# Performance work log

Hardware: AMD Instinct MI355X
Metric: run time of the kernel (lower is better)

The kernel has to match this reference:

```python
import jax, jax.numpy as jnp
import numpy as np

N_VARS = 2_000_000
N_CONSTRS = 1_000_000
NNZ = 20_000_000  # ~20 nonzeros per constraint


def setup_inputs() -> dict:
    key = jax.random.key(0)
    k = jax.random.split(key, 6)
    pred = jax.random.normal(k[0], (N_VARS,), dtype=jnp.float32)
    constr_idx = jax.random.randint(k[1], (NNZ,), 0, N_CONSTRS)
    var_idx = jax.random.randint(k[2], (NNZ,), 0, N_VARS)
    coeff = jax.random.normal(k[3], (NNZ,), dtype=jnp.float32)
    constr_rhs = jax.random.normal(k[4], (N_CONSTRS,), dtype=jnp.float32)
    # sense: 1 = <=, 2 = >=, 3 = ==
    constr_sense = jax.random.randint(k[5], (N_CONSTRS,), 1, 4)
    return {
        "pred": pred,
        "constr_idx": constr_idx,
        "var_idx": var_idx,
        "coeff": coeff,
        "constr_rhs": constr_rhs,
        "constr_sense": constr_sense,
        "n_vars": N_VARS,
        "n_constrs": N_CONSTRS,
    }


def reference(pred, constr_idx, var_idx, coeff, constr_rhs, constr_sense, n_vars, n_constrs):
    # var_types is None -> all binary: values = sigmoid(pred)
    values = jax.nn.sigmoid(pred)
    # COO sparse matvec: ax[c] = sum over nonzeros with constr_idx==c of coeff * values[var_idx]
    ax = jax.ops.segment_sum(coeff * values[var_idx], constr_idx, num_segments=n_constrs)
    diff = ax - constr_rhs
    zero = jnp.zeros((), dtype=diff.dtype)
    violations = jnp.where(
        constr_sense == 1, jnp.maximum(diff, zero),          # <= : relu(ax - b)
        jnp.where(
            constr_sense == 2, jnp.maximum(-diff, zero),     # >= : relu(b - ax)
            jnp.where(constr_sense == 3, jnp.abs(diff), zero)  # == : |ax - b|
        ),
    )
    return violations.mean()  # reduction='mean'
```

## Files before the change

kernel.cpp:

```cpp
#include <hip/hip_runtime.h>
#include <hip/hip_fp16.h>


#define BW_LOG2 13
#define BW (1 << BW_LOG2)
#define MAXNB 128
#define NREP 8
#define P1_THREADS 512
#define VPT 8
#define P1_CHUNK (P1_THREADS * VPT)
#define CUR_PAD 16

typedef int   v4i __attribute__((ext_vector_type(4)));
typedef float v4f __attribute__((ext_vector_type(4)));

__global__ void sigmoid_kernel(const float* __restrict__ pred,
                               __half* __restrict__ values, int n) {
    int i = blockIdx.x * blockDim.x + threadIdx.x;
    int stride = gridDim.x * blockDim.x;
    int n4 = n >> 2;
    const v4f* p4 = (const v4f*)pred;
    uint2* o = (uint2*)values;
    for (int j = i; j < n4; j += stride) {
        v4f p = p4[j];
        float a0 = 1.0f / (1.0f + __expf(-p.x));
        float a1 = 1.0f / (1.0f + __expf(-p.y));
        float a2 = 1.0f / (1.0f + __expf(-p.z));
        float a3 = 1.0f / (1.0f + __expf(-p.w));
        unsigned lo = ((unsigned)__half_as_ushort(__float2half_rn(a1)) << 16) |
                      (unsigned)__half_as_ushort(__float2half_rn(a0));
        unsigned hi = ((unsigned)__half_as_ushort(__float2half_rn(a3)) << 16) |
                      (unsigned)__half_as_ushort(__float2half_rn(a2));
        o[j] = make_uint2(lo, hi);
    }
    for (int j = (n4 << 2) + i; j < n; j += stride)
        values[j] = __float2half_rn(1.0f / (1.0f + __expf(-pred[j])));
}

__global__ __launch_bounds__(P1_THREADS) void binning_kernel(
    const int* __restrict__ cidx, const int* __restrict__ vidx,
    const float* __restrict__ coeff, const __half* __restrict__ values,
    unsigned long long* __restrict__ bins, int* __restrict__ cursor,
    float* __restrict__ ovf, int nnz, int nb, int cap) {
    __shared__ int hist[MAXNB];
    __shared__ int sbase[MAXNB];
    const int tid = threadIdx.x;
    const long long start = (long long)blockIdx.x * P1_CHUNK;

    for (int i = tid; i < nb; i += P1_THREADS) hist[i] = 0;
    __syncthreads();

    unsigned packed[VPT];
    float val[VPT];

    if (start + P1_CHUNK <= (long long)nnz) {
        const v4i* c4 = (const v4i*)(cidx + start);
        const v4i* v4 = (const v4i*)(vidx + start);
        const v4f* w4 = (const v4f*)(coeff + start);
#pragma unroll
        for (int k = 0; k < VPT / 4; ++k) {
            int g = k * P1_THREADS + tid;
            v4i c = __builtin_nontemporal_load(&c4[g]);
            v4i v = __builtin_nontemporal_load(&v4[g]);
            v4f w = __builtin_nontemporal_load(&w4[g]);
            float x0 = w.x * __half2float(values[v.x]);
            float x1 = w.y * __half2float(values[v.y]);
            float x2 = w.z * __half2float(values[v.z]);
            float x3 = w.w * __half2float(values[v.w]);
            int l0 = atomicAdd(&hist[c.x >> BW_LOG2], 1);
            int l1 = atomicAdd(&hist[c.y >> BW_LOG2], 1);
            int l2 = atomicAdd(&hist[c.z >> BW_LOG2], 1);
            int l3 = atomicAdd(&hist[c.w >> BW_LOG2], 1);
            packed[k * 4 + 0] = (unsigned)c.x | ((unsigned)l0 << 20);
            packed[k * 4 + 1] = (unsigned)c.y | ((unsigned)l1 << 20);
            packed[k * 4 + 2] = (unsigned)c.z | ((unsigned)l2 << 20);
            packed[k * 4 + 3] = (unsigned)c.w | ((unsigned)l3 << 20);
            val[k * 4 + 0] = x0;
            val[k * 4 + 1] = x1;
            val[k * 4 + 2] = x2;
            val[k * 4 + 3] = x3;
        }
    } else {
#pragma unroll
        for (int k = 0; k < VPT; ++k) {
            long long idx = start + (long long)k * P1_THREADS + tid;
            if (idx < nnz) {
                int c = cidx[idx];
                float x = coeff[idx] * __half2float(values[vidx[idx]]);
                int l = atomicAdd(&hist[c >> BW_LOG2], 1);
                packed[k] = (unsigned)c | ((unsigned)l << 20);
                val[k] = x;
            } else {
                packed[k] = 0xFFFFFFFFu;
            }
        }
    }
    __syncthreads();
    for (int i = tid; i < nb; i += P1_THREADS)
        sbase[i] = atomicAdd(&cursor[i * CUR_PAD], hist[i]);
    __syncthreads();
#pragma unroll
    for (int k = 0; k < VPT; ++k) {
        if (packed[k] == 0xFFFFFFFFu) continue;
        unsigned c = packed[k] & 0xFFFFFu;
        int loc = (int)(packed[k] >> 20);
        int b = (int)(c >> BW_LOG2);
        int pos = sbase[b] + loc;
        if (pos < cap) {
            unsigned long long e = (unsigned long long)c |
                ((unsigned long long)__float_as_uint(val[k]) << 32);
            bins[(size_t)b * cap + pos] = e;
        } else {
            atomicAdd(&ovf[c], val[k]);
        }
    }
}

__global__ __launch_bounds__(512) void bucket_accum_kernel(
    const unsigned long long* __restrict__ bins, const int* __restrict__ cursor,
    float* __restrict__ rep, int nb, int cap, int n_constrs, int rep_stride) {
    __shared__ float acc[BW];
    const int tid = threadIdx.x;
    const int b = blockIdx.x >> 3;
    const int r = blockIdx.x & 7;

    v4f* a4 = (v4f*)acc;
    v4f zero = {0.0f, 0.0f, 0.0f, 0.0f};
#pragma unroll
    for (int k = 0; k < BW / 4 / 512; ++k)
        a4[k * 512 + tid] = zero;
    __syncthreads();

    int cnt = cursor[b * CUR_PAD];
    if (cnt > cap) cnt = cap;
    int begin = (int)((long long)cnt * r / NREP);
    int end = (int)((long long)cnt * (r + 1) / NREP);
    const unsigned long long* mb = bins + (size_t)b * cap;
    const unsigned cbase = (unsigned)b << BW_LOG2;

    int i = begin + tid;
    for (; i + 512 * 3 < end; i += 512 * 4) {
        unsigned long long e0 = mb[i];
        unsigned long long e1 = mb[i + 512];
        unsigned long long e2 = mb[i + 1024];
        unsigned long long e3 = mb[i + 1536];
        atomicAdd(&acc[((unsigned)e0 & 0xFFFFFu) - cbase], __uint_as_float((unsigned)(e0 >> 32)));
        atomicAdd(&acc[((unsigned)e1 & 0xFFFFFu) - cbase], __uint_as_float((unsigned)(e1 >> 32)));
        atomicAdd(&acc[((unsigned)e2 & 0xFFFFFu) - cbase], __uint_as_float((unsigned)(e2 >> 32)));
        atomicAdd(&acc[((unsigned)e3 & 0xFFFFFu) - cbase], __uint_as_float((unsigned)(e3 >> 32)));
    }
    for (; i < end; i += 512) {
        unsigned long long e = mb[i];
        atomicAdd(&acc[((unsigned)e & 0xFFFFFu) - cbase], __uint_as_float((unsigned)(e >> 32)));
    }
    __syncthreads();

    float* out = rep + (size_t)r * rep_stride + cbase;
    int lim = n_constrs - (int)cbase;
    if (lim >= BW) {
        v4f* o4 = (v4f*)out;
#pragma unroll
        for (int k = 0; k < BW / 4 / 512; ++k)
            o4[k * 512 + tid] = a4[k * 512 + tid];
    } else {
        for (int j = tid; j < lim; j += 512) out[j] = acc[j];
    }
}

template <int NR>
__global__ void violation_reduce_kernel(const float* __restrict__ rep,
                                        const float* __restrict__ rhs,
                                        const int* __restrict__ sense,
                                        float* __restrict__ out,
                                        int n, int rep_stride, float inv_n) {
    int i = blockIdx.x * blockDim.x + threadIdx.x;
    int stride = gridDim.x * blockDim.x;
    float acc = 0.0f;
    int n4 = n >> 2;
    const float4* r4 = (const float4*)rhs;
    const int4* s4 = (const int4*)sense;
    for (int j = i; j < n4; j += stride) {
        float4 a = make_float4(0.0f, 0.0f, 0.0f, 0.0f);
#pragma unroll
        for (int r = 0; r < NR; ++r) {
            const float4* a4 = (const float4*)(rep + (size_t)r * (size_t)rep_stride);
            float4 t = a4[j];
            a.x += t.x; a.y += t.y; a.z += t.z; a.w += t.w;
        }
        float4 rr = r4[j];
        int4 s = s4[j];
        float d;
        d = a.x - rr.x;
        acc += (s.x == 1) ? fmaxf(d, 0.0f) : (s.x == 2) ? fmaxf(-d, 0.0f) : (s.x == 3) ? fabsf(d) : 0.0f;
        d = a.y - rr.y;
        acc += (s.y == 1) ? fmaxf(d, 0.0f) : (s.y == 2) ? fmaxf(-d, 0.0f) : (s.y == 3) ? fabsf(d) : 0.0f;
        d = a.z - rr.z;
        acc += (s.z == 1) ? fmaxf(d, 0.0f) : (s.z == 2) ? fmaxf(-d, 0.0f) : (s.z == 3) ? fabsf(d) : 0.0f;
        d = a.w - rr.w;
        acc += (s.w == 1) ? fmaxf(d, 0.0f) : (s.w == 2) ? fmaxf(-d, 0.0f) : (s.w == 3) ? fabsf(d) : 0.0f;
    }
    for (int j = (n4 << 2) + i; j < n; j += stride) {
        float a = 0.0f;
#pragma unroll
        for (int r = 0; r < NR; ++r) a += rep[(size_t)r * (size_t)rep_stride + j];
        float d = a - rhs[j];
        int s = sense[j];
        acc += (s == 1) ? fmaxf(d, 0.0f) : (s == 2) ? fmaxf(-d, 0.0f) : (s == 3) ? fabsf(d) : 0.0f;
    }

    for (int off = 32; off > 0; off >>= 1)
        acc += __shfl_down(acc, off, 64);

    __shared__ float lds[8];
    int lane = threadIdx.x & 63;
    int wave = threadIdx.x >> 6;
    if (lane == 0) lds[wave] = acc;
    __syncthreads();
    if (wave == 0) {
        int nwaves = blockDim.x >> 6;
        float b = (lane < nwaves) ? lds[lane] : 0.0f;
        for (int off = 4; off > 0; off >>= 1)
            b += __shfl_down(b, off, 64);
        if (lane == 0) atomicAdd(out, b * inv_n);
    }
}

__global__ void scatter_kernel(const int* __restrict__ cidx,
                               const int* __restrict__ vidx,
                               const float* __restrict__ coeff,
                               const __half* __restrict__ values,
                               float* __restrict__ ax, int nnz) {
    int i = blockIdx.x * blockDim.x + threadIdx.x;
    int stride = gridDim.x * blockDim.x;
    int n4 = nnz >> 2;
    const int4* c4 = (const int4*)cidx;
    const int4* v4 = (const int4*)vidx;
    const float4* w4 = (const float4*)coeff;
    for (int j = i; j < n4; j += stride) {
        int4 c = c4[j];
        int4 v = v4[j];
        float4 w = w4[j];
        atomicAdd(&ax[c.x], w.x * __half2float(values[v.x]));
        atomicAdd(&ax[c.y], w.y * __half2float(values[v.y]));
        atomicAdd(&ax[c.z], w.z * __half2float(values[v.z]));
        atomicAdd(&ax[c.w], w.w * __half2float(values[v.w]));
    }
    for (int j = (n4 << 2) + i; j < nnz; j += stride)
        atomicAdd(&ax[cidx[j]], coeff[j] * __half2float(values[vidx[j]]));
}

extern "C" void kernel_launch(void* const* d_in, const int* in_sizes, int n_in,
                              void* d_out, int out_size, void* d_ws, size_t ws_size,
                              hipStream_t stream) {
    const float* pred  = (const float*)d_in[0];
    const int*   cidx  = (const int*)d_in[1];
    const int*   vidx  = (const int*)d_in[2];
    const float* coeff = (const float*)d_in[3];
    const float* rhs   = (const float*)d_in[4];
    const int*   sense = (const int*)d_in[5];

    const int n_vars    = in_sizes[0];
    const int nnz       = in_sizes[1];
    const int n_constrs = in_sizes[4];

    const int rep_stride = (n_constrs + 15) & ~15;
    const size_t vh_bytes = ((size_t)n_vars * 2 + 255) & ~(size_t)255;

    __half* values = (__half*)d_ws;
    float* rep = (float*)((char*)d_ws + vh_bytes);
    float* ovf = rep + (size_t)NREP * rep_stride;
    int* cursor = (int*)(ovf + rep_stride);
    unsigned long long* bins =
        (unsigned long long*)(cursor + MAXNB * CUR_PAD);

    const int nb = (n_constrs + BW - 1) >> BW_LOG2;
    long long cap_ll = (long long)nnz * BW / n_constrs
                     + (long long)nnz / ((long long)(nb > 0 ? nb : 1) * 32) + 2048;
    const int cap = (int)cap_ll;
    const size_t need = vh_bytes
                      + (size_t)(NREP + 1) * rep_stride * 4
                      + (size_t)MAXNB * CUR_PAD * 4
                      + (size_t)nb * (size_t)cap * 8;
    const bool fast = (nb >= 1) && (nb <= MAXNB) && (n_constrs < (1 << 20)) &&
                      (nnz > P1_CHUNK) && (ws_size >= need);

    hipMemsetAsync(d_out, 0, sizeof(float), stream);

    {
        int threads = 256;
        int work = n_vars >> 2;
        int blocks = (work + threads - 1) / threads;
        if (blocks < 1) blocks = 1;
        if (blocks > 2048) blocks = 2048;
        sigmoid_kernel<<<blocks, threads, 0, stream>>>(pred, values, n_vars);
    }

    if (fast) {
        hipMemsetAsync(cursor, 0, (size_t)MAXNB * CUR_PAD * sizeof(int), stream);
        hipMemsetAsync(ovf, 0, (size_t)rep_stride * sizeof(float), stream);

        int p1_blocks = (int)(((long long)nnz + P1_CHUNK - 1) / P1_CHUNK);
        binning_kernel<<<p1_blocks, P1_THREADS, 0, stream>>>(
            cidx, vidx, coeff, values, bins, cursor, ovf, nnz, nb, cap);

        bucket_accum_kernel<<<nb * NREP, 512, 0, stream>>>(
            bins, cursor, rep, nb, cap, n_constrs, rep_stride);

        int threads = 256;
        int work = n_constrs >> 2;
        int blocks = (work + threads - 1) / threads;
        if (blocks > 4096) blocks = 4096;
        violation_reduce_kernel<NREP + 1><<<blocks, threads, 0, stream>>>(
            rep, rhs, sense, (float*)d_out, n_constrs, rep_stride,
            1.0f / (float)n_constrs);
    } else {
        hipMemsetAsync(rep, 0, (size_t)n_constrs * sizeof(float), stream);
        int threads = 256;
        int work = nnz >> 2;
        int blocks = (work + threads - 1) / threads;
        if (blocks > 8192) blocks = 8192;
        scatter_kernel<<<blocks, threads, 0, stream>>>(
            cidx, vidx, coeff, values, rep, nnz);

        int vthreads = 256;
        int vwork = n_constrs >> 2;
        int vblocks = (vwork + vthreads - 1) / vthreads;
        if (vblocks > 4096) vblocks = 4096;
        violation_reduce_kernel<1><<<vblocks, vthreads, 0, stream>>>(
            rep, rhs, sense, (float*)d_out, n_constrs, n_constrs,
            1.0f / (float)n_constrs);
    }
}
```

Baseline: 539.6 us.

## Pack bins to 32-bit half entries and fuse accumulation with violation reduction

Bin entries shrink from 64-bit (constraint index plus fp32 value) to 32-bit (12-bit local index plus fp16 product), halving the scatter and readback traffic of the bin array. Bucket width halves to 4096 and block size doubles to 1024, so each bucket is accumulated by one block in LDS. That block then computes the violations and reduces them directly, which removes the replicated partial-sum buffers and the separate violation kernel. The cost is fewer accumulation blocks (about 245), which may underfill the GPU. Storing each product in fp16 also adds rounding error to every term.

Result: faster. 525.8 us (-2.6%).

```diff
diff --git a/kernel.cpp b/kernel.cpp
--- a/kernel.cpp
+++ b/kernel.cpp
@@ -2,11 +2,10 @@
 #include <hip/hip_fp16.h>
 
 
-#define BW_LOG2 13
+#define BW_LOG2 12
 #define BW (1 << BW_LOG2)
-#define MAXNB 128
-#define NREP 8
-#define P1_THREADS 512
+#define MAXNB 256
+#define P1_THREADS 1024
 #define VPT 8
 #define P1_CHUNK (P1_THREADS * VPT)
 #define CUR_PAD 16
@@ -40,7 +39,7 @@
 __global__ __launch_bounds__(P1_THREADS) void binning_kernel(
     const int* __restrict__ cidx, const int* __restrict__ vidx,
     const float* __restrict__ coeff, const __half* __restrict__ values,
-    unsigned long long* __restrict__ bins, int* __restrict__ cursor,
+    unsigned* __restrict__ bins, int* __restrict__ cursor,
     float* __restrict__ ovf, int nnz, int nb, int cap) {
     __shared__ int hist[MAXNB];
     __shared__ int sbase[MAXNB];
@@ -50,8 +49,9 @@
     for (int i = tid; i < nb; i += P1_THREADS) hist[i] = 0;
     __syncthreads();
 
-    unsigned packed[VPT];
-    float val[VPT];
+    int   cc[VPT];
+    float vv[VPT];
+    int   ll[VPT];
 
     if (start + P1_CHUNK <= (long long)nnz) {
         const v4i* c4 = (const v4i*)(cidx + start);
@@ -63,22 +63,16 @@
             v4i c = __builtin_nontemporal_load(&c4[g]);
             v4i v = __builtin_nontemporal_load(&v4[g]);
             v4f w = __builtin_nontemporal_load(&w4[g]);
-            float x0 = w.x * __half2float(values[v.x]);
-            float x1 = w.y * __half2float(values[v.y]);
-            float x2 = w.z * __half2float(values[v.z]);
-            float x3 = w.w * __half2float(values[v.w]);
-            int l0 = atomicAdd(&hist[c.x >> BW_LOG2], 1);
-            int l1 = atomicAdd(&hist[c.y >> BW_LOG2], 1);
-            int l2 = atomicAdd(&hist[c.z >> BW_LOG2], 1);
-            int l3 = atomicAdd(&hist[c.w >> BW_LOG2], 1);
-            packed[k * 4 + 0] = (unsigned)c.x | ((unsigned)l0 << 20);
-            packed[k * 4 + 1] = (unsigned)c.y | ((unsigned)l1 << 20);
-            packed[k * 4 + 2] = (unsigned)c.z | ((unsigned)l2 << 20);
-            packed[k * 4 + 3] = (unsigned)c.w | ((unsigned)l3 << 20);
-            val[k * 4 + 0] = x0;
-            val[k * 4 + 1] = x1;
-            val[k * 4 + 2] = x2;
-            val[k * 4 + 3] = x3;
+            vv[k * 4 + 0] = w.x * __half2float(values[v.x]);
+            vv[k * 4 + 1] = w.y * __half2float(values[v.y]);
+            vv[k * 4 + 2] = w.z * __half2float(values[v.z]);
+            vv[k * 4 + 3] = w.w * __half2float(values[v.w]);
+            cc[k * 4 + 0] = c.x; cc[k * 4 + 1] = c.y;
+            cc[k * 4 + 2] = c.z; cc[k * 4 + 3] = c.w;
+            ll[k * 4 + 0] = atomicAdd(&hist[c.x >> BW_LOG2], 1);
+            ll[k * 4 + 1] = atomicAdd(&hist[c.y >> BW_LOG2], 1);
+            ll[k * 4 + 2] = atomicAdd(&hist[c.z >> BW_LOG2], 1);
+            ll[k * 4 + 3] = atomicAdd(&hist[c.w >> BW_LOG2], 1);
         }
     } else {
 #pragma unroll
@@ -86,12 +80,11 @@
             long long idx = start + (long long)k * P1_THREADS + tid;
             if (idx < nnz) {
                 int c = cidx[idx];
-                float x = coeff[idx] * __half2float(values[vidx[idx]]);
-                int l = atomicAdd(&hist[c >> BW_LOG2], 1);
-                packed[k] = (unsigned)c | ((unsigned)l << 20);
-                val[k] = x;
+                cc[k] = c;
+                vv[k] = coeff[idx] * __half2float(values[vidx[idx]]);
+                ll[k] = atomicAdd(&hist[c >> BW_LOG2], 1);
             } else {
-                packed[k] = 0xFFFFFFFFu;
+                cc[k] = -1;
             }
         }
     }
@@ -101,127 +94,88 @@
     __syncthreads();
 #pragma unroll
     for (int k = 0; k < VPT; ++k) {
-        if (packed[k] == 0xFFFFFFFFu) continue;
-        unsigned c = packed[k] & 0xFFFFFu;
-        int loc = (int)(packed[k] >> 20);
-        int b = (int)(c >> BW_LOG2);
-        int pos = sbase[b] + loc;
+        int c = cc[k];
+        if (c < 0) continue;
+        int b = c >> BW_LOG2;
+        int pos = sbase[b] + ll[k];
         if (pos < cap) {
-            unsigned long long e = (unsigned long long)c |
-                ((unsigned long long)__float_as_uint(val[k]) << 32);
-            bins[(size_t)b * cap + pos] = e;
+            unsigned short hb = __half_as_ushort(__float2half_rn(vv[k]));
+            bins[(size_t)b * cap + pos] =
+                ((unsigned)hb << 16) | (unsigned)(c & (BW - 1));
         } else {
-            atomicAdd(&ovf[c], val[k]);
+            atomicAdd(&ovf[c], vv[k]);
         }
     }
 }
 
-__global__ __launch_bounds__(512) void bucket_accum_kernel(
-    const unsigned long long* __restrict__ bins, const int* __restrict__ cursor,
-    float* __restrict__ rep, int nb, int cap, int n_constrs, int rep_stride) {
+__global__ __launch_bounds__(1024) void accum_viol_kernel(
+    const unsigned* __restrict__ bins, const int* __restrict__ cursor,
+    const float* __restrict__ ovf, const float* __restrict__ rhs,
+    const int* __restrict__ sense, float* __restrict__ out,
+    int cap, int n_constrs, float inv_n) {
     __shared__ float acc[BW];
     const int tid = threadIdx.x;
-    const int b = blockIdx.x >> 3;
-    const int r = blockIdx.x & 7;
-
-    v4f* a4 = (v4f*)acc;
-    v4f zero = {0.0f, 0.0f, 0.0f, 0.0f};
-#pragma unroll
-    for (int k = 0; k < BW / 4 / 512; ++k)
-        a4[k * 512 + tid] = zero;
+    const int b = blockIdx.x;
+
+#pragma unroll
+    for (int k = 0; k < BW / 1024; ++k) acc[k * 1024 + tid] = 0.0f;
     __syncthreads();
 
     int cnt = cursor[b * CUR_PAD];
     if (cnt > cap) cnt = cap;
-    int begin = (int)((long long)cnt * r / NREP);
-    int end = (int)((long long)cnt * (r + 1) / NREP);
-    const unsigned long long* mb = bins + (size_t)b * cap;
-    const unsigned cbase = (unsigned)b << BW_LOG2;
-
-    int i = begin + tid;
-    for (; i + 512 * 3 < end; i += 512 * 4) {
-        unsigned long long e0 = mb[i];
-        unsigned long long e1 = mb[i + 512];
-        unsigned long long e2 = mb[i + 1024];
-        unsigned long long e3 = mb[i + 1536];
-        atomicAdd(&acc[((unsigned)e0 & 0xFFFFFu) - cbase], __uint_as_float((unsigned)(e0 >> 32)));
-        atomicAdd(&acc[((unsigned)e1 & 0xFFFFFu) - cbase], __uint_as_float((unsigned)(e1 >> 32)));
-        atomicAdd(&acc[((unsigned)e2 & 0xFFFFFu) - cbase], __uint_as_float((unsigned)(e2 >> 32)));
-        atomicAdd(&acc[((unsigned)e3 & 0xFFFFFu) - cbase], __uint_as_float((unsigned)(e3 >> 32)));
-    }
-    for (; i < end; i += 512) {
-        unsigned long long e = mb[i];
-        atomicAdd(&acc[((unsigned)e & 0xFFFFFu) - cbase], __uint_as_float((unsigned)(e >> 32)));
-    }
-    __syncthreads();
-
-    float* out = rep + (size_t)r * rep_stride + cbase;
-    int lim = n_constrs - (int)cbase;
-    if (lim >= BW) {
-        v4f* o4 = (v4f*)out;
-#pragma unroll
-        for (int k = 0; k < BW / 4 / 512; ++k)
-            o4[k * 512 + tid] = a4[k * 512 + tid];
-    } else {
-        for (int j = tid; j < lim; j += 512) out[j] = acc[j];
-    }
-}
-
-template <int NR>
-__global__ void violation_reduce_kernel(const float* __restrict__ rep,
-                                        const float* __restrict__ rhs,
-                                        const int* __restrict__ sense,
-                                        float* __restrict__ out,
-                                        int n, int rep_stride, float inv_n) {
-    int i = blockIdx.x * blockDim.x + threadIdx.x;
-    int stride = gridDim.x * blockDim.x;
-    float acc = 0.0f;
-    int n4 = n >> 2;
-    const float4* r4 = (const float4*)rhs;
-    const int4* s4 = (const int4*)sense;
-    for (int j = i; j < n4; j += stride) {
-        float4 a = make_float4(0.0f, 0.0f, 0.0f, 0.0f);
-#pragma unroll
-        for (int r = 0; r < NR; ++r) {
-            const float4* a4 = (const float4*)(rep + (size_t)r * (size_t)rep_stride);
-            float4 t = a4[j];
-            a.x += t.x; a.y += t.y; a.z += t.z; a.w += t.w;
+    const unsigned* mb = bins + (size_t)b * cap;
+
+    int i = tid;
+    for (; i + 1024 * 3 < cnt; i += 1024 * 4) {
+        unsigned e0 = __builtin_nontemporal_load(&mb[i]);
+        unsigned e1 = __builtin_nontemporal_load(&mb[i + 1024]);
+        unsigned e2 = __builtin_nontemporal_load(&mb[i + 2048]);
+        unsigned e3 = __builtin_nontemporal_load(&mb[i + 3072]);
+        atomicAdd(&acc[e0 & (BW - 1)],
+                  __half2float(__ushort_as_half((unsigned short)(e0 >> 16))));
+        atomicAdd(&acc[e1 & (BW - 1)],
+                  __half2float(__ushort_as_half((unsigned short)(e1 >> 16))));
+        atomicAdd(&acc[e2 & (BW - 1)],
+                  __half2float(__ushort_as_half((unsigned short)(e2 >> 16))));
+        atomicAdd(&acc[e3 & (BW - 1)],
+                  __half2float(__ushort_as_half((unsigned short)(e3 >> 16))));
+    }
+    for (; i < cnt; i += 1024) {
+        unsigned e = __builtin_nontemporal_load(&mb[i]);
+        atomicAdd(&acc[e & (BW - 1)],
+                  __half2float(__ushort_as_half((unsigned short)(e >> 16))));
+    }
+    __syncthreads();
+
+    const int cbase = b << BW_LOG2;
+    float sum = 0.0f;
+#pragma unroll
+    for (int k = 0; k < BW / 1024; ++k) {
+        int j = k * 1024 + tid;
+        int c = cbase + j;
+        if (c < n_constrs) {
+            float a = acc[j] + ovf[c];
+            float d = a - rhs[c];
+            int s = sense[c];
+            sum += (s == 1) ? fmaxf(d, 0.0f)
+                 : (s == 2) ? fmaxf(-d, 0.0f)
+                 : (s == 3) ? fabsf(d) : 0.0f;
         }
-        float4 rr = r4[j];
-        int4 s = s4[j];
-        float d;
-        d = a.x - rr.x;
-        acc += (s.x == 1) ? fmaxf(d, 0.0f) : (s.x == 2) ? fmaxf(-d, 0.0f) : (s.x == 3) ? fabsf(d) : 0.0f;
-        d = a.y - rr.y;
-        acc += (s.y == 1) ? fmaxf(d, 0.0f) : (s.y == 2) ? fmaxf(-d, 0.0f) : (s.y == 3) ? fabsf(d) : 0.0f;
-        d = a.z - rr.z;
-        acc += (s.z == 1) ? fmaxf(d, 0.0f) : (s.z == 2) ? fmaxf(-d, 0.0f) : (s.z == 3) ? fabsf(d) : 0.0f;
-        d = a.w - rr.w;
-        acc += (s.w == 1) ? fmaxf(d, 0.0f) : (s.w == 2) ? fmaxf(-d, 0.0f) : (s.w == 3) ? fabsf(d) : 0.0f;
-    }
-    for (int j = (n4 << 2) + i; j < n; j += stride) {
-        float a = 0.0f;
-#pragma unroll
-        for (int r = 0; r < NR; ++r) a += rep[(size_t)r * (size_t)rep_stride + j];
-        float d = a - rhs[j];
-        int s = sense[j];
-        acc += (s == 1) ? fmaxf(d, 0.0f) : (s == 2) ? fmaxf(-d, 0.0f) : (s == 3) ? fabsf(d) : 0.0f;
     }
 
     for (int off = 32; off > 0; off >>= 1)
-        acc += __shfl_down(acc, off, 64);
-
-    __shared__ float lds[8];
-    int lane = threadIdx.x & 63;
-    int wave = threadIdx.x >> 6;
-    if (lane == 0) lds[wave] = acc;
+        sum += __shfl_down(sum, off, 64);
+
+    __shared__ float lds[16];
+    int lane = tid & 63;
+    int wave = tid >> 6;
+    if (lane == 0) lds[wave] = sum;
     __syncthreads();
     if (wave == 0) {
-        int nwaves = blockDim.x >> 6;
-        float b = (lane < nwaves) ? lds[lane] : 0.0f;
-        for (int off = 4; off > 0; off >>= 1)
-            b += __shfl_down(b, off, 64);
-        if (lane == 0) atomicAdd(out, b * inv_n);
+        float v = (lane < 16) ? lds[lane] : 0.0f;
+        for (int off = 8; off > 0; off >>= 1)
+            v += __shfl_down(v, off, 64);
+        if (lane == 0) atomicAdd(out, v * inv_n);
     }
 }
 
@@ -249,6 +203,36 @@
         atomicAdd(&ax[cidx[j]], coeff[j] * __half2float(values[vidx[j]]));
 }
 
+__global__ void violation_reduce_kernel(const float* __restrict__ ax,
+                                        const float* __restrict__ rhs,
+                                        const int* __restrict__ sense,
+                                        float* __restrict__ out,
+                                        int n, float inv_n) {
+    int i = blockIdx.x * blockDim.x + threadIdx.x;
+    int stride = gridDim.x * blockDim.x;
+    float acc = 0.0f;
+    for (int j = i; j < n; j += stride) {
+        float d = ax[j] - rhs[j];
+        int s = sense[j];
+        acc += (s == 1) ? fmaxf(d, 0.0f) : (s == 2) ? fmaxf(-d, 0.0f)
+             : (s == 3) ? fabsf(d) : 0.0f;
+    }
+    for (int off = 32; off > 0; off >>= 1)
+        acc += __shfl_down(acc, off, 64);
+    __shared__ float lds[8];
+    int lane = threadIdx.x & 63;
+    int wave = threadIdx.x >> 6;
+    if (lane == 0) lds[wave] = acc;
+    __syncthreads();
+    if (wave == 0) {
+        int nwaves = blockDim.x >> 6;
+        float b = (lane < nwaves) ? lds[lane] : 0.0f;
+        for (int off = 4; off > 0; off >>= 1)
+            b += __shfl_down(b, off, 64);
+        if (lane == 0) atomicAdd(out, b * inv_n);
+    }
+}
+
 extern "C" void kernel_launch(void* const* d_in, const int* in_sizes, int n_in,
                               void* d_out, int out_size, void* d_ws, size_t ws_size,
                               hipStream_t stream) {
@@ -263,26 +247,23 @@
     const int nnz       = in_sizes[1];
     const int n_constrs = in_sizes[4];
 
-    const int rep_stride = (n_constrs + 15) & ~15;
     const size_t vh_bytes = ((size_t)n_vars * 2 + 255) & ~(size_t)255;
+    const size_t ovf_bytes = (((size_t)n_constrs * 4) + 255) & ~(size_t)255;
 
     __half* values = (__half*)d_ws;
-    float* rep = (float*)((char*)d_ws + vh_bytes);
-    float* ovf = rep + (size_t)NREP * rep_stride;
-    int* cursor = (int*)(ovf + rep_stride);
-    unsigned long long* bins =
-        (unsigned long long*)(cursor + MAXNB * CUR_PAD);
+    float* ovf = (float*)((char*)d_ws + vh_bytes);
+    int* cursor = (int*)((char*)ovf + ovf_bytes);
+    unsigned* bins = (unsigned*)(cursor + MAXNB * CUR_PAD);
 
     const int nb = (n_constrs + BW - 1) >> BW_LOG2;
-    long long cap_ll = (long long)nnz * BW / n_constrs
-                     + (long long)nnz / ((long long)(nb > 0 ? nb : 1) * 32) + 2048;
+    long long cap_ll = (long long)nnz / (nb > 0 ? nb : 1)
+                     + (long long)nnz / ((long long)(nb > 0 ? nb : 1) * 16) + 4096;
     const int cap = (int)cap_ll;
-    const size_t need = vh_bytes
-                      + (size_t)(NREP + 1) * rep_stride * 4
+    const size_t need = vh_bytes + ovf_bytes
                       + (size_t)MAXNB * CUR_PAD * 4
-                      + (size_t)nb * (size_t)cap * 8;
-    const bool fast = (nb >= 1) && (nb <= MAXNB) && (n_constrs < (1 << 20)) &&
-                      (nnz > P1_CHUNK) && (ws_size >= need);
+                      + (size_t)nb * (size_t)cap * 4;
+    const bool fast = (nb >= 1) && (nb <= MAXNB) && (n_constrs <= (1 << 20)) &&
+                      (nnz > 0) && (ws_size >= need);
 
     hipMemsetAsync(d_out, 0, sizeof(float), stream);
 
@@ -297,37 +278,30 @@
 
     if (fast) {
         hipMemsetAsync(cursor, 0, (size_t)MAXNB * CUR_PAD * sizeof(int), stream);
-        hipMemsetAsync(ovf, 0, (size_t)rep_stride * sizeof(float), stream);
+        hipMemsetAsync(ovf, 0, (size_t)n_constrs * sizeof(float), stream);
 
         int p1_blocks = (int)(((long long)nnz + P1_CHUNK - 1) / P1_CHUNK);
         binning_kernel<<<p1_blocks, P1_THREADS, 0, stream>>>(
             cidx, vidx, coeff, values, bins, cursor, ovf, nnz, nb, cap);
 
-        bucket_accum_kernel<<<nb * NREP, 512, 0, stream>>>(
-            bins, cursor, rep, nb, cap, n_constrs, rep_stride);
-
-        int threads = 256;
-        int work = n_constrs >> 2;
-        int blocks = (work + threads - 1) / threads;
-        if (blocks > 4096) blocks = 4096;
-        violation_reduce_kernel<NREP + 1><<<blocks, threads, 0, stream>>>(
-            rep, rhs, sense, (float*)d_out, n_constrs, rep_stride,
-            1.0f / (float)n_constrs);
+        accum_viol_kernel<<<nb, 1024, 0, stream>>>(
+            bins, cursor, ovf, rhs, sense, (float*)d_out,
+            cap, n_constrs, 1.0f / (float)n_constrs);
     } else {
-        hipMemsetAsync(rep, 0, (size_t)n_constrs * sizeof(float), stream);
+        hipMemsetAsync(ovf, 0, (size_t)n_constrs * sizeof(float), stream);
         int threads = 256;
         int work = nnz >> 2;
         int blocks = (work + threads - 1) / threads;
+        if (blocks < 1) blocks = 1;
         if (blocks > 8192) blocks = 8192;
         scatter_kernel<<<blocks, threads, 0, stream>>>(
-            cidx, vidx, coeff, values, rep, nnz);
+            cidx, vidx, coeff, values, ovf, nnz);
 
         int vthreads = 256;
-        int vwork = n_constrs >> 2;
-        int vblocks = (vwork + vthreads - 1) / vthreads;
+        int vblocks = (n_constrs + vthreads - 1) / vthreads;
         if (vblocks > 4096) vblocks = 4096;
-        violation_reduce_kernel<1><<<vblocks, vthreads, 0, stream>>>(
-            rep, rhs, sense, (float*)d_out, n_constrs, n_constrs,
+        violation_reduce_kernel<<<vblocks, vthreads, 0, stream>>>(
+            ovf, rhs, sense, (float*)d_out, n_constrs,
             1.0f / (float)n_constrs);
     }
 }
```
